# Kernel tuning notes

Hardware: AMD Instinct MI355X
Metric: run time of the kernel (lower is better)

Reference implementation:

```python
import jax, jax.numpy as jnp
import numpy as np

MSE_WEIGHT = 1.0
PHYSICS_WEIGHT = 0.1
VAR_IDX = np.array([2, 1, 0, 3, 4])
VAR_W = np.array([0.5, 0.15, 0.15, 0.1, 0.1], dtype=np.float32)
TEMP_IDX = np.array([5, 7, 8, 9, 11])
TEMP_W = 0.1
TEMP_THRESH = 5.0


def setup_inputs() -> dict:
    key = jax.random.key(0)
    k1, k2, k3, k4, k5 = jax.random.split(key, 5)
    B, S, W, D = 524288, 4, 8, 16
    return {
        "pred": jax.random.normal(k1, (B, S, D), dtype=jnp.float32),
        "target": jax.random.normal(k2, (B, S, D), dtype=jnp.float32),
        "input_sequence": jax.random.normal(k3, (B, W, D), dtype=jnp.float32),
        "scale": jax.random.uniform(k4, (D,), dtype=jnp.float32, minval=0.5, maxval=2.0),
        "mean": jax.random.normal(k5, (D,), dtype=jnp.float32),
    }


def reference(pred, target, input_sequence, scale, mean):
    B, S, D = pred.shape
    # step weights: 1/(k+1), normalized
    step_w = 1.0 / (jnp.arange(S, dtype=jnp.float32) + 1.0)
    step_w = step_w / jnp.sum(step_w)

    # --- weighted per-variable MSE (gradients flow through pred/target) ---
    var_idx = jnp.asarray(VAR_IDX)
    var_w = jnp.asarray(VAR_W)
    diff2 = (pred[:, :, var_idx] - target[:, :, var_idx]) ** 2  # [B, S, 5]
    mse_per_step = jnp.einsum("bsv,v->s", diff2, var_w) / B      # [S]
    mse_loss = jnp.dot(step_w, mse_per_step)

    # --- physics terms on detached, de-normalized states ---
    pred_sg = jax.lax.stop_gradient(pred)
    prev = jnp.concatenate(
        [jax.lax.stop_gradient(input_sequence[:, -1:, :]), pred_sg[:, :-1, :]], axis=1
    )  # [B, S, D]
    pd = pred_sg * scale + mean   # inverse_transform (StandardScaler)
    pv = prev * scale + mean

    air, water = pd[:, :, 3], pd[:, :, 4]
    heat_balance = jnp.mean((air - water) ** 2, axis=0) / (jnp.mean(air ** 2, axis=0) + 1e-6)  # [S]

    frost_dec = jax.nn.relu(pv[:, :, 2] - pd[:, :, 2])
    frost_mono = jnp.mean(frost_dec ** 2, axis=0)  # [S]

    press_dec = jax.nn.relu(pv[:, :, 0] - pd[:, :, 0]) * 0.5
    press_growth = jnp.mean(press_dec ** 2, axis=0)  # [S]

    tidx = jnp.asarray(TEMP_IDX)
    temp_diff = jnp.abs(pd[:, :, tidx] - pv[:, :, tidx])            # [B, S, 5]
    temp_pen = TEMP_W * jnp.sum(jnp.mean(jax.nn.relu(temp_diff - TEMP_THRESH) ** 2, axis=0), axis=-1)  # [S]

    physics_per_step = heat_balance + frost_mono + press_growth + temp_pen  # [S]
    physics_loss = jnp.dot(step_w, physics_per_step)

    return MSE_WEIGHT * mse_loss + PHYSICS_WEIGHT * physics_loss
```

## Files before the change

kernel.cpp:

```cpp
#include <hip/hip_runtime.h>

#define B_TOTAL 524288
#define TILE_B 128
#define NBLK (B_TOTAL / TILE_B)
#define NTHR 512


__device__ __forceinline__ void gload_lds16(const void* g, void* l) {
    __builtin_amdgcn_global_load_lds(
        (const __attribute__((address_space(1))) void*)g,
        (__attribute__((address_space(3))) void*)l, 16, 0, 0);
}

__global__ __launch_bounds__(NTHR) void loss_partial(
    const float* __restrict__ pred,
    const float* __restrict__ target,
    const float* __restrict__ inseq,
    const float* __restrict__ scale,
    const float* __restrict__ mean,
    float* __restrict__ partials)
{
    __shared__ float4 sp[TILE_B * 12];
    __shared__ float4 st[TILE_B * 8];

    const int tid = threadIdx.x;
    const size_t tile0 = (size_t)blockIdx.x * TILE_B;

    const float4* prg = reinterpret_cast<const float4*>(pred) + tile0 * 16;
    const float4* tgg = reinterpret_cast<const float4*>(target) + tile0 * 16;

#pragma unroll
    for (int it = 0; it < 3; ++it) {
        int j = it * NTHR + tid;
        int i = j ^ ((j >> 3) & 7);
        int r = i / 3, k = i - r * 3;
        gload_lds16(prg + r * 4 + k, sp + j);
    }
#pragma unroll
    for (int it = 0; it < 2; ++it) {
        int j = it * NTHR + tid;
        int i = j ^ ((j >> 3) & 7);
        gload_lds16(tgg + ((i >> 1) << 2) + (i & 1), st + j);
    }

    const int b = tid >> 2;
    const int s = tid & 3;

    float pv0 = 0.f, pv2 = 0.f, pv5 = 0.f, pv7 = 0.f, pv8 = 0.f, pv9 = 0.f, pv11 = 0.f;
    if (s == 0) {
        const float4* iq = reinterpret_cast<const float4*>(inseq + (tile0 + (size_t)b) * 128 + 112);
        float4 q0 = iq[0], q1 = iq[1], q2 = iq[2];
        pv0 = q0.x; pv2 = q0.z; pv5 = q1.y; pv7 = q1.w;
        pv8 = q2.x; pv9 = q2.y; pv11 = q2.w;
    }

    const float sc0 = scale[0], sc2 = scale[2], sc3 = scale[3], sc4 = scale[4];
    const float sc5 = scale[5], sc7 = scale[7], sc8 = scale[8], sc9 = scale[9], sc11 = scale[11];
    const float mn3 = mean[3], mn4 = mean[4];
    const float sw = (s == 0) ? 0.48f : (s == 1) ? 0.24f : (s == 2) ? 0.16f : 0.12f;

    __syncthreads();

    auto ldp = [&](int row, int w) -> float4 {
        int i = row * 3 + w;
        return sp[i ^ ((i >> 3) & 7)];
    };
    auto ldt = [&](int row, int h) -> float4 {
        int i = row * 2 + h;
        return st[i ^ ((i >> 3) & 7)];
    };

    const int row = b * 4 + s;
    if (s != 0) {
        float4 q0 = ldp(row - 1, 0), q1 = ldp(row - 1, 1), q2 = ldp(row - 1, 2);
        pv0 = q0.x; pv2 = q0.z; pv5 = q1.y; pv7 = q1.w;
        pv8 = q2.x; pv9 = q2.y; pv11 = q2.w;
    }

    float4 p0 = ldp(row, 0), p1 = ldp(row, 1), p2 = ldp(row, 2);
    float4 t0 = ldt(row, 0), t1 = ldt(row, 1);

    float d0 = p0.x - t0.x, d1 = p0.y - t0.y, d2 = p0.z - t0.z;
    float d3 = p0.w - t0.w, d4 = p1.x - t1.x;
    float acc_mse = sw * (0.15f * d0 * d0 + 0.15f * d1 * d1 + 0.5f * d2 * d2 +
                          0.1f * d3 * d3 + 0.1f * d4 * d4);

    float air = p0.w * sc3 + mn3;
    float water = p1.x * sc4 + mn4;
    float hdf = air - water;
    float hn = hdf * hdf;
    float hd = air * air;

    float fr = fmaxf((pv2 - p0.z) * sc2, 0.f);
    float pg = fmaxf((pv0 - p0.x) * sc0, 0.f) * 0.5f;
    float rest = fr * fr + pg * pg;
    float t5 = fmaxf(fabsf(p1.y - pv5) * sc5 - 5.f, 0.f);
    float t7 = fmaxf(fabsf(p1.w - pv7) * sc7 - 5.f, 0.f);
    float t8 = fmaxf(fabsf(p2.x - pv8) * sc8 - 5.f, 0.f);
    float t9 = fmaxf(fabsf(p2.y - pv9) * sc9 - 5.f, 0.f);
    float t11 = fmaxf(fabsf(p2.w - pv11) * sc11 - 5.f, 0.f);
    rest += 0.1f * (t5 * t5 + t7 * t7 + t8 * t8 + t9 * t9 + t11 * t11);
    float acc_rest = sw * rest;

    __syncthreads();

    const int lane = tid & 63;
    const int wave = tid >> 6;
#pragma unroll
    for (int off = 1; off < 64; off <<= 1) {
        acc_mse  += __shfl_xor(acc_mse, off, 64);
        acc_rest += __shfl_xor(acc_rest, off, 64);
    }
#pragma unroll
    for (int off = 4; off < 64; off <<= 1) {
        hn += __shfl_xor(hn, off, 64);
        hd += __shfl_xor(hd, off, 64);
    }

    float* red = reinterpret_cast<float*>(st);
    if (lane == 0) { red[wave * 10 + 0] = acc_mse; red[wave * 10 + 1] = acc_rest; }
    if (lane < 4)  { red[wave * 10 + 2 + lane] = hn; red[wave * 10 + 6 + lane] = hd; }
    __syncthreads();

    if (tid < 10) {
        float v = 0.f;
#pragma unroll
        for (int w = 0; w < 8; ++w) v += red[w * 10 + tid];
        partials[tid * NBLK + blockIdx.x] = v;
    }
}

__global__ __launch_bounds__(640) void loss_final(
    const float* __restrict__ partials,
    float* __restrict__ out)
{
    __shared__ float tot[10];
    const int t = threadIdx.x;
    const int c = t >> 6;
    const int lane = t & 63;

    float v = 0.f;
#pragma unroll
    for (int i = 0; i < NBLK / 64; ++i)
        v += partials[(size_t)c * NBLK + i * 64 + lane];
#pragma unroll
    for (int off = 32; off; off >>= 1) v += __shfl_down(v, off, 64);
    if (lane == 0) tot[c] = v;
    __syncthreads();

    if (t == 0) {
        const float stepw[4] = {0.48f, 0.24f, 0.16f, 0.12f};
        const float invB = 1.0f / (float)B_TOTAL;
        float mse = tot[0] * invB;
        float phys = tot[1] * invB;
#pragma unroll
        for (int s = 0; s < 4; ++s) {
            float num = tot[2 + s] * invB;
            float den = tot[6 + s] * invB + 1e-6f;
            phys += stepw[s] * (num / den);
        }
        out[0] = mse + 0.1f * phys;
    }
}

extern "C" void kernel_launch(void* const* d_in, const int* in_sizes, int n_in,
                              void* d_out, int out_size, void* d_ws, size_t ws_size,
                              hipStream_t stream) {
    const float* pred   = (const float*)d_in[0];
    const float* target = (const float*)d_in[1];
    const float* inseq  = (const float*)d_in[2];
    const float* scale  = (const float*)d_in[3];
    const float* mean   = (const float*)d_in[4];
    float* out = (float*)d_out;
    float* partials = (float*)d_ws;

    loss_partial<<<NBLK, NTHR, 0, stream>>>(pred, target, inseq, scale, mean, partials);
    loss_final<<<1, 640, 0, stream>>>(partials, out);
}
```

Before: 61.83 us.

## Make partial-loss kernel persistent over eight tiles with double-buffered LDS prefetch

Each block now processes eight 128-row tiles instead of one. Loads for the next tile go into a second LDS buffer through global_load_lds while the current tile is computed, using manual vmcnt waits and s_barriers. This amortizes per-block setup and the reduction, cuts the number of partials, and overlaps memory latency with compute. In exchange it doubles LDS use, which may lower occupancy, and the hand-written waitcnt accounting has to match the number of outstanding loads per thread exactly.

```diff
diff --git a/kernel.cpp b/kernel.cpp
--- a/kernel.cpp
+++ b/kernel.cpp
@@ -2,11 +2,12 @@
 
 #define B_TOTAL 524288
 #define TILE_B 128
-#define NBLK (B_TOTAL / TILE_B)
+#define TPB 8
+#define GRID (B_TOTAL / (TILE_B * TPB))
 #define NTHR 512
 
 
-__device__ __forceinline__ void gload_lds16(const void* g, void* l) {
+__device__ __forceinline__ void gload_lds16(const float4* g, float4* l) {
     __builtin_amdgcn_global_load_lds(
         (const __attribute__((address_space(1))) void*)g,
         (__attribute__((address_space(3))) void*)l, 16, 0, 0);
@@ -20,89 +21,109 @@
     const float* __restrict__ mean,
     float* __restrict__ partials)
 {
-    __shared__ float4 sp[TILE_B * 12];
-    __shared__ float4 st[TILE_B * 8];
+    __shared__ float4 sp[2][TILE_B * 12];
+    __shared__ float4 st[2][TILE_B * 8];
 
     const int tid = threadIdx.x;
-    const size_t tile0 = (size_t)blockIdx.x * TILE_B;
-
-    const float4* prg = reinterpret_cast<const float4*>(pred) + tile0 * 16;
-    const float4* tgg = reinterpret_cast<const float4*>(target) + tile0 * 16;
-
-#pragma unroll
-    for (int it = 0; it < 3; ++it) {
-        int j = it * NTHR + tid;
-        int i = j ^ ((j >> 3) & 7);
-        int r = i / 3, k = i - r * 3;
-        gload_lds16(prg + r * 4 + k, sp + j);
-    }
-#pragma unroll
-    for (int it = 0; it < 2; ++it) {
-        int j = it * NTHR + tid;
-        int i = j ^ ((j >> 3) & 7);
-        gload_lds16(tgg + ((i >> 1) << 2) + (i & 1), st + j);
-    }
-
     const int b = tid >> 2;
     const int s = tid & 3;
+    const int row = tid;
+    const size_t blk0 = (size_t)blockIdx.x * (TPB * TILE_B);
 
-    float pv0 = 0.f, pv2 = 0.f, pv5 = 0.f, pv7 = 0.f, pv8 = 0.f, pv9 = 0.f, pv11 = 0.f;
-    if (s == 0) {
-        const float4* iq = reinterpret_cast<const float4*>(inseq + (tile0 + (size_t)b) * 128 + 112);
-        float4 q0 = iq[0], q1 = iq[1], q2 = iq[2];
-        pv0 = q0.x; pv2 = q0.z; pv5 = q1.y; pv7 = q1.w;
-        pv8 = q2.x; pv9 = q2.y; pv11 = q2.w;
-    }
+    const float4* prg = reinterpret_cast<const float4*>(pred) + blk0 * 16;
+    const float4* tgg = reinterpret_cast<const float4*>(target) + blk0 * 16;
+    const float4* iqg = reinterpret_cast<const float4*>(inseq) + blk0 * 32 + (size_t)b * 32 + 28;
+
+    int po0, po1, po2, to0, to1;
+    { int j = tid;        int i = j ^ ((j >> 3) & 7); int r = i / 3; po0 = r * 4 + (i - r * 3); }
+    { int j = 512 + tid;  int i = j ^ ((j >> 3) & 7); int r = i / 3; po1 = r * 4 + (i - r * 3); }
+    { int j = 1024 + tid; int i = j ^ ((j >> 3) & 7); int r = i / 3; po2 = r * 4 + (i - r * 3); }
+    { int j = tid;        int i = j ^ ((j >> 3) & 7); to0 = ((i >> 1) << 2) | (i & 1); }
+    { int j = 512 + tid;  int i = j ^ ((j >> 3) & 7); to1 = ((i >> 1) << 2) | (i & 1); }
 
     const float sc0 = scale[0], sc2 = scale[2], sc3 = scale[3], sc4 = scale[4];
     const float sc5 = scale[5], sc7 = scale[7], sc8 = scale[8], sc9 = scale[9], sc11 = scale[11];
     const float mn3 = mean[3], mn4 = mean[4];
     const float sw = (s == 0) ? 0.48f : (s == 1) ? 0.24f : (s == 2) ? 0.16f : 0.12f;
 
-    __syncthreads();
-
-    auto ldp = [&](int row, int w) -> float4 {
-        int i = row * 3 + w;
-        return sp[i ^ ((i >> 3) & 7)];
+    auto STAGE = [&](int bi, int t) {
+        const float4* pg = prg + (size_t)t * (TILE_B * 16);
+        const float4* tg = tgg + (size_t)t * (TILE_B * 16);
+        gload_lds16(pg + po0, &sp[bi][tid]);
+        gload_lds16(pg + po1, &sp[bi][512 + tid]);
+        gload_lds16(pg + po2, &sp[bi][1024 + tid]);
+        gload_lds16(tg + to0, &st[bi][tid]);
+        gload_lds16(tg + to1, &st[bi][512 + tid]);
     };
-    auto ldt = [&](int row, int h) -> float4 {
-        int i = row * 2 + h;
-        return st[i ^ ((i >> 3) & 7)];
+    auto LOADQ = [&](float4* q, int t) {
+        if (s == 0) {
+            const float4* iq = iqg + (size_t)t * (TILE_B * 32);
+            q[0] = iq[0]; q[1] = iq[1]; q[2] = iq[2];
+        }
     };
 
-    const int row = b * 4 + s;
-    if (s != 0) {
-        float4 q0 = ldp(row - 1, 0), q1 = ldp(row - 1, 1), q2 = ldp(row - 1, 2);
-        pv0 = q0.x; pv2 = q0.z; pv5 = q1.y; pv7 = q1.w;
-        pv8 = q2.x; pv9 = q2.y; pv11 = q2.w;
+    float acc_mse = 0.f, acc_rest = 0.f, hn = 0.f, hd = 0.f;
+
+    auto COMPUTE = [&](int bi, const float4* q) {
+        auto ldp = [&](int rr, int w) -> float4 {
+            int i = rr * 3 + w; return sp[bi][i ^ ((i >> 3) & 7)];
+        };
+        auto ldt = [&](int rr, int h) -> float4 {
+            int i = rr * 2 + h; return st[bi][i ^ ((i >> 3) & 7)];
+        };
+        float pv0, pv2, pv5, pv7, pv8, pv9, pv11;
+        if (s != 0) {
+            float4 a0 = ldp(row - 1, 0), a1 = ldp(row - 1, 1), a2 = ldp(row - 1, 2);
+            pv0 = a0.x; pv2 = a0.z; pv5 = a1.y; pv7 = a1.w;
+            pv8 = a2.x; pv9 = a2.y; pv11 = a2.w;
+        } else {
+            pv0 = q[0].x; pv2 = q[0].z; pv5 = q[1].y; pv7 = q[1].w;
+            pv8 = q[2].x; pv9 = q[2].y; pv11 = q[2].w;
+        }
+        float4 p0 = ldp(row, 0), p1 = ldp(row, 1), p2 = ldp(row, 2);
+        float4 t0 = ldt(row, 0), t1 = ldt(row, 1);
+
+        float d0 = p0.x - t0.x, d1 = p0.y - t0.y, d2 = p0.z - t0.z;
+        float d3 = p0.w - t0.w, d4 = p1.x - t1.x;
+        acc_mse += sw * (0.15f * d0 * d0 + 0.15f * d1 * d1 + 0.5f * d2 * d2 +
+                         0.1f * d3 * d3 + 0.1f * d4 * d4);
+        float air = p0.w * sc3 + mn3;
+        float water = p1.x * sc4 + mn4;
+        float hdf = air - water;
+        hn += hdf * hdf;
+        hd += air * air;
+        float fr = fmaxf((pv2 - p0.z) * sc2, 0.f);
+        float pg2 = fmaxf((pv0 - p0.x) * sc0, 0.f) * 0.5f;
+        float rest = fr * fr + pg2 * pg2;
+        float t5 = fmaxf(fabsf(p1.y - pv5) * sc5 - 5.f, 0.f);
+        float t7 = fmaxf(fabsf(p1.w - pv7) * sc7 - 5.f, 0.f);
+        float t8 = fmaxf(fabsf(p2.x - pv8) * sc8 - 5.f, 0.f);
+        float t9 = fmaxf(fabsf(p2.y - pv9) * sc9 - 5.f, 0.f);
+        float t11 = fmaxf(fabsf(p2.w - pv11) * sc11 - 5.f, 0.f);
+        rest += 0.1f * (t5 * t5 + t7 * t7 + t8 * t8 + t9 * t9 + t11 * t11);
+        acc_rest += sw * rest;
+    };
+
+    float4 qreg[2][3];
+
+    STAGE(0, 0);
+    LOADQ(qreg[0], 0);
+#pragma unroll
+    for (int t = 0; t < TPB; ++t) {
+        const int cur = t & 1, nxt = (t + 1) & 1;
+        if (t > 0) {
+            asm volatile("s_barrier" ::: "memory");
+        }
+        if (t + 1 < TPB) {
+            STAGE(nxt, t + 1);
+            LOADQ(qreg[nxt], t + 1);
+            asm volatile("s_waitcnt vmcnt(8)" ::: "memory");
+        } else {
+            asm volatile("s_waitcnt vmcnt(0)" ::: "memory");
+        }
+        asm volatile("s_barrier" ::: "memory");
+        COMPUTE(cur, qreg[cur]);
     }
-
-    float4 p0 = ldp(row, 0), p1 = ldp(row, 1), p2 = ldp(row, 2);
-    float4 t0 = ldt(row, 0), t1 = ldt(row, 1);
-
-    float d0 = p0.x - t0.x, d1 = p0.y - t0.y, d2 = p0.z - t0.z;
-    float d3 = p0.w - t0.w, d4 = p1.x - t1.x;
-    float acc_mse = sw * (0.15f * d0 * d0 + 0.15f * d1 * d1 + 0.5f * d2 * d2 +
-                          0.1f * d3 * d3 + 0.1f * d4 * d4);
-
-    float air = p0.w * sc3 + mn3;
-    float water = p1.x * sc4 + mn4;
-    float hdf = air - water;
-    float hn = hdf * hdf;
-    float hd = air * air;
-
-    float fr = fmaxf((pv2 - p0.z) * sc2, 0.f);
-    float pg = fmaxf((pv0 - p0.x) * sc0, 0.f) * 0.5f;
-    float rest = fr * fr + pg * pg;
-    float t5 = fmaxf(fabsf(p1.y - pv5) * sc5 - 5.f, 0.f);
-    float t7 = fmaxf(fabsf(p1.w - pv7) * sc7 - 5.f, 0.f);
-    float t8 = fmaxf(fabsf(p2.x - pv8) * sc8 - 5.f, 0.f);
-    float t9 = fmaxf(fabsf(p2.y - pv9) * sc9 - 5.f, 0.f);
-    float t11 = fmaxf(fabsf(p2.w - pv11) * sc11 - 5.f, 0.f);
-    rest += 0.1f * (t5 * t5 + t7 * t7 + t8 * t8 + t9 * t9 + t11 * t11);
-    float acc_rest = sw * rest;
-
-    __syncthreads();
 
     const int lane = tid & 63;
     const int wave = tid >> 6;
@@ -116,8 +137,7 @@
         hn += __shfl_xor(hn, off, 64);
         hd += __shfl_xor(hd, off, 64);
     }
-
-    float* red = reinterpret_cast<float*>(st);
+    float* red = reinterpret_cast<float*>(&st[0][0]);
     if (lane == 0) { red[wave * 10 + 0] = acc_mse; red[wave * 10 + 1] = acc_rest; }
     if (lane < 4)  { red[wave * 10 + 2 + lane] = hn; red[wave * 10 + 6 + lane] = hd; }
     __syncthreads();
@@ -126,7 +146,7 @@
         float v = 0.f;
 #pragma unroll
         for (int w = 0; w < 8; ++w) v += red[w * 10 + tid];
-        partials[tid * NBLK + blockIdx.x] = v;
+        partials[tid * GRID + blockIdx.x] = v;
     }
 }
 
@@ -141,8 +161,8 @@
 
     float v = 0.f;
 #pragma unroll
-    for (int i = 0; i < NBLK / 64; ++i)
-        v += partials[(size_t)c * NBLK + i * 64 + lane];
+    for (int i = 0; i < GRID / 64; ++i)
+        v += partials[(size_t)c * GRID + i * 64 + lane];
 #pragma unroll
     for (int off = 32; off; off >>= 1) v += __shfl_down(v, off, 64);
     if (lane == 0) tot[c] = v;
@@ -154,10 +174,10 @@
         float mse = tot[0] * invB;
         float phys = tot[1] * invB;
 #pragma unroll
-        for (int s = 0; s < 4; ++s) {
-            float num = tot[2 + s] * invB;
-            float den = tot[6 + s] * invB + 1e-6f;
-            phys += stepw[s] * (num / den);
+        for (int q = 0; q < 4; ++q) {
+            float num = tot[2 + q] * invB;
+            float den = tot[6 + q] * invB + 1e-6f;
+            phys += stepw[q] * (num / den);
         }
         out[0] = mse + 0.1f * phys;
     }
@@ -174,6 +194,6 @@
     float* out = (float*)d_out;
     float* partials = (float*)d_ws;
 
-    loss_partial<<<NBLK, NTHR, 0, stream>>>(pred, target, inseq, scale, mean, partials);
+    loss_partial<<<GRID, NTHR, 0, stream>>>(pred, target, inseq, scale, mean, partials);
     loss_final<<<1, 640, 0, stream>>>(partials, out);
 }
```

Result: slower. 69.63 us (+12.6%).
